# Performance work log

Measured on AMD Instinct MI355X. Metric: run time of the kernel, lower is better.

The kernel has to match this reference:

```python
import jax, jax.numpy as jnp
import numpy as np

WS = 11      # window_size
SIGMA = 1.5
CH = 4       # channels / groups (hardcoded in forward)
SCALE = 1.0


def _gaussian_window(dtype):
    x = np.arange(WS, dtype=np.float64) - WS // 2
    g = np.exp(-(x ** 2) / (2.0 * SIGMA ** 2))
    g = g / g.sum()
    w2 = np.outer(g, g).astype(np.float32)          # [WS, WS]
    w = np.broadcast_to(w2, (CH, 1, WS, WS)).copy()  # [O, I/groups, kH, kW]
    return jnp.asarray(w, dtype=dtype)


def _dwconv(x, w):
    # depthwise conv2d, groups=CH, VALID padding (matches F.conv2d default padding=0)
    return jax.lax.conv_general_dilated(
        x, w, window_strides=(1, 1), padding='VALID',
        dimension_numbers=('NCHW', 'OIHW', 'NCHW'),
        feature_group_count=CH)


def setup_inputs() -> dict:
    key = jax.random.key(0)
    k1, k2 = jax.random.split(key)
    X = jax.random.normal(k1, (16, 4, 512, 512), dtype=jnp.float32)
    Y = jax.random.normal(k2, (16, 4, 512, 512), dtype=jnp.float32)
    return {"X": X, "Y": Y}


def reference(X, Y):
    w = _gaussian_window(X.dtype)
    muX = _dwconv(X, w)
    muY = _dwconv(Y, w)
    muX_sq, muY_sq, muXY = muX * muX, muY * muY, muX * muY
    sigmaX_sq = _dwconv(X * X, w) - muX_sq
    sigmaY_sq = _dwconv(Y * Y, w) - muY_sq
    sigmaXY = _dwconv(X * Y, w) - muXY
    C1 = (0.01 * SCALE) ** 2
    C2 = (0.03 * SCALE) ** 2
    v1 = 2.0 * sigmaXY + C2
    v2 = sigmaX_sq + sigmaY_sq + C2
    ssim_map = (2.0 * muXY + C1) * v1 / ((muX_sq + muY_sq + C1) * v2)
    return 1.0 - ssim_map.mean()
```

## Files before the change

kernel.cpp:

```cpp
#include <hip/hip_runtime.h>
#include <hip/hip_bf16.h>
#include <cmath>


#define IMG   512
#define ODIM  502
#define SC    16
#define BR    128
#define WPB   4
#define BC    (SC * WPB)
#define GX    8
#define GY    4
#define NC    64
#define NBLK  (GX * GY * NC)

typedef float          f32x4  __attribute__((ext_vector_type(4)));
typedef __bf16         bf16x8 __attribute__((ext_vector_type(8)));
typedef __bf16         bf16x4 __attribute__((ext_vector_type(4)));
typedef short          s16x4  __attribute__((ext_vector_type(4)));
typedef unsigned int   u32x2  __attribute__((ext_vector_type(2)));
typedef unsigned int   u32x4  __attribute__((ext_vector_type(4)));

union F8 { bf16x8 v; __bf16 b[8]; u32x4 q; };
union F4 { bf16x4 v; s16x4 s; __bf16 b[4]; u32x2 q; };

__device__ __forceinline__ unsigned short bfbits(float f) {
    __bf16 h = (__bf16)f;
    return __builtin_bit_cast(unsigned short, h);
}

__device__ __forceinline__ f32x4 mfma16(const F4& a, const F4& b, f32x4 c) {
    return __builtin_amdgcn_mfma_f32_16x16x16bf16_1k(a.s, b.s, c, 0, 0, 0);
}

struct GaussW { float g[11]; };

__global__ __launch_bounds__(256, 4) void ssim_mfma_kernel(
    const float* __restrict__ X, const float* __restrict__ Y,
    float* __restrict__ partial, GaussW gw)
{
    __shared__ unsigned short wl[16][40];
    __shared__ float wsum[WPB];

    const int tid  = threadIdx.x;
    const int lane = tid & 63;
    const int wave = tid >> 6;
    const int m    = lane & 15;
    const int g    = lane >> 4;

    for (int t = tid; t < 16 * 40; t += 256) {
        const int mm = t / 40, kk = t - 40 * mm;
        const int d  = kk - mm;
        wl[mm][kk] = bfbits((kk < 32 && d >= 0 && d < 11) ? gw.g[d] : 0.f);
    }
    __syncthreads();

    const int gx0 = blockIdx.x * BC + SC * wave;
    const int gy0 = blockIdx.y * BR;
    const int nc  = blockIdx.z;
    const float* __restrict__ Xp = X + (size_t)nc * IMG * IMG;
    const float* __restrict__ Yp = Y + (size_t)nc * IMG * IMG;

    F8 wf;  wf.q  = *(const u32x4*)&wl[m][8 * g];
    F4 wa0; wa0.q = *(const u32x2*)&wl[m][4 * g];
    F4 wa1; wa1.q = *(const u32x2*)&wl[m][16 + 4 * g];
    const f32x4 z = {0.f, 0.f, 0.f, 0.f};

    const int cs = min(gx0 + 8 * g, IMG - 8);
    const float* __restrict__ xbase = Xp + (gy0 + m) * IMG + cs;
    const float* __restrict__ ybase = Yp + (gy0 + m) * IMG + cs;

    auto mfmaH = [&](F4 (&hd)[5], f32x4 a0, f32x4 a1, f32x4 b0, f32x4 b1) {
        const f32x4 xx0 = a0 * a0, xx1 = a1 * a1;
        const f32x4 yy0 = b0 * b0, yy1 = b1 * b1;
        const f32x4 xy0 = a0 * b0, xy1 = a1 * b1;
        F8 fx, fy, fxx, fyy, fxy;
#pragma unroll
        for (int j = 0; j < 4; ++j) {
            fx.b[j]      = (__bf16)a0[j];
            fx.b[4 + j]  = (__bf16)a1[j];
            fy.b[j]      = (__bf16)b0[j];
            fy.b[4 + j]  = (__bf16)b1[j];
            fxx.b[j]     = (__bf16)xx0[j];
            fxx.b[4 + j] = (__bf16)xx1[j];
            fyy.b[j]     = (__bf16)yy0[j];
            fyy.b[4 + j] = (__bf16)yy1[j];
            fxy.b[j]     = (__bf16)xy0[j];
            fxy.b[4 + j] = (__bf16)xy1[j];
        }
        const f32x4 dX  = __builtin_amdgcn_mfma_f32_16x16x32_bf16(fx.v,  wf.v, z, 0, 0, 0);
        const f32x4 dY  = __builtin_amdgcn_mfma_f32_16x16x32_bf16(fy.v,  wf.v, z, 0, 0, 0);
        const f32x4 dXX = __builtin_amdgcn_mfma_f32_16x16x32_bf16(fxx.v, wf.v, z, 0, 0, 0);
        const f32x4 dYY = __builtin_amdgcn_mfma_f32_16x16x32_bf16(fyy.v, wf.v, z, 0, 0, 0);
        const f32x4 dXY = __builtin_amdgcn_mfma_f32_16x16x32_bf16(fxy.v, wf.v, z, 0, 0, 0);
#pragma unroll
        for (int i = 0; i < 4; ++i) {
            hd[0].b[i] = (__bf16)dX[i];
            hd[1].b[i] = (__bf16)dY[i];
            hd[2].b[i] = (__bf16)dXX[i];
            hd[3].b[i] = (__bf16)dYY[i];
            hd[4].b[i] = (__bf16)dXY[i];
        }
    };

    f32x4 vacc = z;
    const int gxv   = gx0 + m;
    const bool colok = (gxv < ODIM);

    auto vstage = [&](const F4 (&h0)[5], const F4 (&h1)[5], int vt) {
        f32x4 e[5];
#pragma unroll
        for (int q = 0; q < 5; ++q) {
            e[q] = mfma16(wa1, h1[q], z);
            e[q] = mfma16(wa0, h0[q], e[q]);
        }
        const float C1 = 1e-4f, C2 = 9e-4f;
        const f32x4 mX = e[0], mY = e[1];
        const f32x4 muXX = mX * mX;
        const f32x4 muYY = mY * mY;
        const f32x4 muXY = mX * mY;
        const f32x4 sXX = e[2] - muXX;
        const f32x4 sYY = e[3] - muYY;
        const f32x4 sXY = e[4] - muXY;
        const f32x4 num = (2.f * muXY + C1) * (2.f * sXY + C2);
        const f32x4 den = (muXX + muYY + C1) * (sXX + sYY + C2);
        f32x4 val;
#pragma unroll
        for (int i = 0; i < 4; ++i) val[i] = __fdividef(num[i], den[i]);
        const int gyb = gy0 + 16 * vt + 4 * g;
#pragma unroll
        for (int i = 0; i < 4; ++i)
            vacc[i] += (colok && (gyb + i < ODIM)) ? val[i] : 0.f;
    };

    f32x4 xA0, xA1, yA0, yA1;
    f32x4 xB0, xB1, yB0, yB1;
    f32x4 xC0, xC1, yC0, yC1;
    F4 h0[5], h1[5], h2[5];

#define LOADRAW(rt, X0, X1, Y0, Y1) do {                                   \
        const float* xr_;  const float* yr_;                               \
        if ((rt) < 8) {                                                    \
            xr_ = xbase + (rt) * 16 * IMG;                                 \
            yr_ = ybase + (rt) * 16 * IMG;                                 \
        } else {                                                           \
            const int gy_ = min(gy0 + 16 * (rt) + m, IMG - 1);             \
            xr_ = Xp + gy_ * IMG + cs;                                     \
            yr_ = Yp + gy_ * IMG + cs;                                     \
        }                                                                  \
        X0 = *(const f32x4*)xr_;  X1 = *(const f32x4*)(xr_ + 4);           \
        Y0 = *(const f32x4*)yr_;  Y1 = *(const f32x4*)(yr_ + 4);           \
    } while (0)
#define SB __builtin_amdgcn_sched_barrier(0)

    LOADRAW(0, xA0, xA1, yA0, yA1);
    LOADRAW(1, xB0, xB1, yB0, yB1);
    SB;
    LOADRAW(2, xC0, xC1, yC0, yC1);  SB;  mfmaH(h0, xA0, xA1, yA0, yA1);
    LOADRAW(3, xA0, xA1, yA0, yA1);  SB;  mfmaH(h1, xB0, xB1, yB0, yB1);
    LOADRAW(4, xB0, xB1, yB0, yB1);  SB;  mfmaH(h2, xC0, xC1, yC0, yC1);  vstage(h0, h1, 0);
    LOADRAW(5, xC0, xC1, yC0, yC1);  SB;  mfmaH(h0, xA0, xA1, yA0, yA1);  vstage(h1, h2, 1);
    LOADRAW(6, xA0, xA1, yA0, yA1);  SB;  mfmaH(h1, xB0, xB1, yB0, yB1);  vstage(h2, h0, 2);
    LOADRAW(7, xB0, xB1, yB0, yB1);  SB;  mfmaH(h2, xC0, xC1, yC0, yC1);  vstage(h0, h1, 3);
    LOADRAW(8, xC0, xC1, yC0, yC1);  SB;  mfmaH(h0, xA0, xA1, yA0, yA1);  vstage(h1, h2, 4);
    mfmaH(h1, xB0, xB1, yB0, yB1);  vstage(h2, h0, 5);
    mfmaH(h2, xC0, xC1, yC0, yC1);  vstage(h0, h1, 6);
    vstage(h1, h2, 7);
#undef SB
#undef LOADRAW

    float acc = (vacc[0] + vacc[1]) + (vacc[2] + vacc[3]);
#pragma unroll
    for (int off = 32; off > 0; off >>= 1)
        acc += __shfl_down(acc, off, 64);

    if (lane == 0) wsum[wave] = acc;
    __syncthreads();
    if (tid == 0) {
        const float tsum = (wsum[0] + wsum[1]) + (wsum[2] + wsum[3]);
        partial[((size_t)blockIdx.z * gridDim.y + blockIdx.y) * gridDim.x + blockIdx.x] = tsum;
    }
}

__global__ __launch_bounds__(512) void ssim_finish_kernel(
    const float* __restrict__ partial, float* __restrict__ out)
{
    __shared__ double sd[512];
    const float4* p4 = (const float4*)partial;
    const float4 v = p4[threadIdx.x];
    double local = ((double)v.x + (double)v.y) + ((double)v.z + (double)v.w);
    sd[threadIdx.x] = local;
    __syncthreads();
    for (int s = 256; s > 0; s >>= 1) {
        if (threadIdx.x < s) sd[threadIdx.x] += sd[threadIdx.x + s];
        __syncthreads();
    }
    if (threadIdx.x == 0) {
        const double cnt = (double)NC * (double)ODIM * (double)ODIM;
        out[0] = (float)(1.0 - sd[0] / cnt);
    }
}

extern "C" void kernel_launch(void* const* d_in, const int* in_sizes, int n_in,
                              void* d_out, int out_size, void* d_ws, size_t ws_size,
                              hipStream_t stream) {
    const float* X = (const float*)d_in[0];
    const float* Y = (const float*)d_in[1];
    float* out = (float*)d_out;
    float* partial = (float*)d_ws;

    GaussW gw;
    {
        double gd[11], s = 0.0;
        for (int i = 0; i < 11; ++i) {
            const double x = (double)(i - 5);
            gd[i] = std::exp(-(x * x) / (2.0 * 1.5 * 1.5));
            s += gd[i];
        }
        for (int i = 0; i < 11; ++i) gw.g[i] = (float)(gd[i] / s);
    }

    dim3 grid(GX, GY, NC);
    ssim_mfma_kernel<<<grid, 256, 0, stream>>>(X, Y, partial, gw);
    ssim_finish_kernel<<<1, 512, 0, stream>>>(partial, out);
}
```

Baseline: 45.36 us.

## Split row tiles into two interleaved streams and drop sched barriers

```diff
diff --git a/kernel.cpp b/kernel.cpp
--- a/kernel.cpp
+++ b/kernel.cpp
@@ -35,7 +35,7 @@
 
 struct GaussW { float g[11]; };
 
-__global__ __launch_bounds__(256, 4) void ssim_mfma_kernel(
+__global__ __launch_bounds__(256, 3) void ssim_mfma_kernel(
     const float* __restrict__ X, const float* __restrict__ Y,
     float* __restrict__ partial, GaussW gw)
 {
@@ -133,10 +133,11 @@
             vacc[i] += (colok && (gyb + i < ODIM)) ? val[i] : 0.f;
     };
 
-    f32x4 xA0, xA1, yA0, yA1;
-    f32x4 xB0, xB1, yB0, yB1;
-    f32x4 xC0, xC1, yC0, yC1;
-    F4 h0[5], h1[5], h2[5];
+    f32x4 pxa0, pxa1, pya0, pya1;
+    f32x4 pxb0, pxb1, pyb0, pyb1;
+    f32x4 qxa0, qxa1, qya0, qya1;
+    f32x4 qxb0, qxb1, qyb0, qyb1;
+    F4 hp0[5], hp1[5], hq0[5], hq1[5];
 
 #define LOADRAW(rt, X0, X1, Y0, Y1) do {                                   \
         const float* xr_;  const float* yr_;                               \
@@ -151,22 +152,36 @@
         X0 = *(const f32x4*)xr_;  X1 = *(const f32x4*)(xr_ + 4);           \
         Y0 = *(const f32x4*)yr_;  Y1 = *(const f32x4*)(yr_ + 4);           \
     } while (0)
-#define SB __builtin_amdgcn_sched_barrier(0)
-
-    LOADRAW(0, xA0, xA1, yA0, yA1);
-    LOADRAW(1, xB0, xB1, yB0, yB1);
-    SB;
-    LOADRAW(2, xC0, xC1, yC0, yC1);  SB;  mfmaH(h0, xA0, xA1, yA0, yA1);
-    LOADRAW(3, xA0, xA1, yA0, yA1);  SB;  mfmaH(h1, xB0, xB1, yB0, yB1);
-    LOADRAW(4, xB0, xB1, yB0, yB1);  SB;  mfmaH(h2, xC0, xC1, yC0, yC1);  vstage(h0, h1, 0);
-    LOADRAW(5, xC0, xC1, yC0, yC1);  SB;  mfmaH(h0, xA0, xA1, yA0, yA1);  vstage(h1, h2, 1);
-    LOADRAW(6, xA0, xA1, yA0, yA1);  SB;  mfmaH(h1, xB0, xB1, yB0, yB1);  vstage(h2, h0, 2);
-    LOADRAW(7, xB0, xB1, yB0, yB1);  SB;  mfmaH(h2, xC0, xC1, yC0, yC1);  vstage(h0, h1, 3);
-    LOADRAW(8, xC0, xC1, yC0, yC1);  SB;  mfmaH(h0, xA0, xA1, yA0, yA1);  vstage(h1, h2, 4);
-    mfmaH(h1, xB0, xB1, yB0, yB1);  vstage(h2, h0, 5);
-    mfmaH(h2, xC0, xC1, yC0, yC1);  vstage(h0, h1, 6);
-    vstage(h1, h2, 7);
-#undef SB
+
+    LOADRAW(0, pxa0, pxa1, pya0, pya1);
+    LOADRAW(4, qxa0, qxa1, qya0, qya1);
+    LOADRAW(1, pxb0, pxb1, pyb0, pyb1);
+    LOADRAW(5, qxb0, qxb1, qyb0, qyb1);
+    mfmaH(hp0, pxa0, pxa1, pya0, pya1);
+    mfmaH(hq0, qxa0, qxa1, qya0, qya1);
+
+    LOADRAW(2, pxa0, pxa1, pya0, pya1);
+    LOADRAW(6, qxa0, qxa1, qya0, qya1);
+    mfmaH(hp1, pxb0, pxb1, pyb0, pyb1);
+    mfmaH(hq1, qxb0, qxb1, qyb0, qyb1);
+    vstage(hp0, hp1, 0);
+    vstage(hq0, hq1, 4);
+    LOADRAW(3, pxb0, pxb1, pyb0, pyb1);
+    LOADRAW(7, qxb0, qxb1, qyb0, qyb1);
+    mfmaH(hp0, pxa0, pxa1, pya0, pya1);
+    mfmaH(hq0, qxa0, qxa1, qya0, qya1);
+    vstage(hp1, hp0, 1);
+    vstage(hq1, hq0, 5);
+    LOADRAW(4, pxa0, pxa1, pya0, pya1);
+    LOADRAW(8, qxa0, qxa1, qya0, qya1);
+    mfmaH(hp1, pxb0, pxb1, pyb0, pyb1);
+    mfmaH(hq1, qxb0, qxb1, qyb0, qyb1);
+    vstage(hp0, hp1, 2);
+    vstage(hq0, hq1, 6);
+    mfmaH(hp0, pxa0, pxa1, pya0, pya1);
+    mfmaH(hq0, qxa0, qxa1, qya0, qya1);
+    vstage(hp1, hp0, 3);
+    vstage(hq1, hq0, 7);
 #undef LOADRAW
 
     float acc = (vacc[0] + vacc[1]) + (vacc[2] + vacc[3]);
```

Result: slower. 49.50 us (+9.1%).
